# Performance work log

Measured on AMD Instinct MI355X. Metric: run time of the kernel, lower is better.

The kernel has to match this reference:

```python
import jax, jax.numpy as jnp
import numpy as np

B, T = 1024, 128
F_DIM, Z_DIM, TXT_DIM, H = 1024, 256, 768, 8
EPS = 1e-5


def layer_norm(x, g, b):
    mu = jnp.mean(x, axis=-1, keepdims=True)
    var = jnp.var(x, axis=-1, keepdims=True)
    return (x - mu) * jax.lax.rsqrt(var + EPS) * g + b


def setup_inputs() -> dict:
    key = jax.random.key(0)
    ks = jax.random.split(key, 16)
    s = lambda fi, fo: 1.0 / np.sqrt(fi)  # rough init scale
    inp = {
        "x": jax.random.normal(ks[0], (B, F_DIM), jnp.float32),
        "z": jax.random.normal(ks[1], (B, Z_DIM), jnp.float32),
        "text_feat": jax.random.normal(ks[2], (B, T, TXT_DIM), jnp.float32),
        "attention": jnp.ones((B, T), jnp.int32),
        # FiLM
        "Wg": jax.random.normal(ks[3], (F_DIM, Z_DIM), jnp.float32) * s(Z_DIM, F_DIM),
        "bg": jnp.zeros((F_DIM,), jnp.float32),
        "Wb": jax.random.normal(ks[4], (F_DIM, Z_DIM), jnp.float32) * s(Z_DIM, F_DIM),
        "bb": jnp.zeros((F_DIM,), jnp.float32),
        # Linear block (linear -> LayerNorm)
        "Wl": jax.random.normal(ks[5], (F_DIM, F_DIM), jnp.float32) * s(F_DIM, F_DIM),
        "bl": jnp.zeros((F_DIM,), jnp.float32),
        "ln1_g": jnp.ones((F_DIM,), jnp.float32),
        "ln1_b": jnp.zeros((F_DIM,), jnp.float32),
        # cross attention projections
        "Wq": jax.random.normal(ks[6], (F_DIM, F_DIM), jnp.float32) * s(F_DIM, F_DIM),
        "bq": jnp.zeros((F_DIM,), jnp.float32),
        "Wk": jax.random.normal(ks[7], (F_DIM, TXT_DIM), jnp.float32) * s(TXT_DIM, F_DIM),
        "bk": jnp.zeros((F_DIM,), jnp.float32),
        "Wv": jax.random.normal(ks[8], (F_DIM, TXT_DIM), jnp.float32) * s(TXT_DIM, F_DIM),
        "bv": jnp.zeros((F_DIM,), jnp.float32),
        "Wo": jax.random.normal(ks[9], (F_DIM, F_DIM), jnp.float32) * s(F_DIM, F_DIM),
        "bo": jnp.zeros((F_DIM,), jnp.float32),
        # post-attention LayerNorm
        "ln2_g": jnp.ones((F_DIM,), jnp.float32),
        "ln2_b": jnp.zeros((F_DIM,), jnp.float32),
    }
    return inp


def reference(x, z, text_feat, attention, Wg, bg, Wb, bb, Wl, bl, ln1_g, ln1_b,
              Wq, bq, Wk, bk, Wv, bv, Wo, bo, ln2_g, ln2_b):
    d = F_DIM // H
    # FiLM params from condition z
    gamma = z @ Wg.T + bg            # [B, F]
    beta = z @ Wb.T + bb             # [B, F]
    # Linear block: linear -> LayerNorm (dropout p=0, identity activation)
    out = layer_norm(x @ Wl.T + bl, ln1_g, ln1_b)
    out = out * (1.0 + gamma) + beta  # FiLM modulation
    # single-query multi-head cross attention
    q = (out @ Wq.T + bq).reshape(B, H, d)                 # [B, H, d] (query len 1)
    k = (text_feat @ Wk.T + bk).reshape(B, T, H, d)         # [B, T, H, d]
    v = (text_feat @ Wv.T + bv).reshape(B, T, H, d)
    scores = jnp.einsum("bhd,bthd->bht", q, k) / jnp.sqrt(jnp.float32(d))  # [B, H, T]
    mask = (attention[:, None, :] != 0)                     # [B, 1, T]
    scores = jnp.where(mask, scores, -jnp.inf)
    attn = jax.nn.softmax(scores, axis=-1)                  # [B, H, T]
    ctx = jnp.einsum("bht,bthd->bhd", attn, v).reshape(B, F_DIM)
    attn_out = ctx @ Wo.T + bo
    out = out + layer_norm(attn_out, ln2_g, ln2_b)
    return jax.nn.gelu(out, approximate=False)
```

## Files before the change

### kernel.cpp

```cpp
#include <hip/hip_runtime.h>

#define EPS 1e-5f

typedef __bf16 bf16x8 __attribute__((ext_vector_type(8)));
typedef float f32x4 __attribute__((ext_vector_type(4)));
typedef ushort ushort8 __attribute__((ext_vector_type(8)));

static __device__ __forceinline__ ushort f2bf(float x) {
    union { float f; unsigned u; } v; v.f = x;
    unsigned r = v.u + 0x7fffu + ((v.u >> 16) & 1u);
    return (ushort)(r >> 16);
}
static __device__ __forceinline__ float bf2f(ushort u) {
    union { unsigned u32; float f; } v; v.u32 = (unsigned)u << 16;
    return v.f;
}

template<int OB>
__global__ __launch_bounds__(256)
void gemm_bb(const ushort* __restrict__ A, int lda, int Aoffz,
             const ushort* __restrict__ W, int ldw, int Woffz,
             void* __restrict__ Cv, int ldc, int Coffz,
             const float* __restrict__ bias, int boffz,
             float scale, int K)
{
    const int z = blockIdx.z;
    A += (size_t)z * Aoffz;
    W += (size_t)z * Woffz;
    const int bm = blockIdx.y * 64, bn = blockIdx.x * 64;

    __shared__ ushort As[64][72];
    __shared__ ushort Bs[64][72];

    const int tid  = threadIdx.x;
    const int lane = tid & 63, wv = tid >> 6;
    const int wm = (wv >> 1) * 32, wn = (wv & 1) * 32;

    const int srow = tid >> 2;
    const int scol = (tid & 3) * 16;
    const ushort* Agp = A + (size_t)(bm + srow) * lda + scol;
    const ushort* Wgp = W + (size_t)(bn + srow) * ldw + scol;

    const int fr = lane & 15, fk = (lane >> 4) * 8;

    f32x4 acc[2][2] = {};

    ushort8 a0 = *(const ushort8*)(Agp);
    ushort8 a1 = *(const ushort8*)(Agp + 8);
    ushort8 b0 = *(const ushort8*)(Wgp);
    ushort8 b1 = *(const ushort8*)(Wgp + 8);

    for (int kt = 0; kt < K; kt += 64) {
        *(ushort8*)&As[srow][scol]     = a0;
        *(ushort8*)&As[srow][scol + 8] = a1;
        *(ushort8*)&Bs[srow][scol]     = b0;
        *(ushort8*)&Bs[srow][scol + 8] = b1;
        __syncthreads();
        if (kt + 64 < K) {
            a0 = *(const ushort8*)(Agp + kt + 64);
            a1 = *(const ushort8*)(Agp + kt + 64 + 8);
            b0 = *(const ushort8*)(Wgp + kt + 64);
            b1 = *(const ushort8*)(Wgp + kt + 64 + 8);
        }
        #pragma unroll
        for (int ks = 0; ks < 64; ks += 32) {
            bf16x8 af0 = *(const bf16x8*)&As[wm + fr][ks + fk];
            bf16x8 af1 = *(const bf16x8*)&As[wm + 16 + fr][ks + fk];
            bf16x8 bf0 = *(const bf16x8*)&Bs[wn + fr][ks + fk];
            bf16x8 bf1 = *(const bf16x8*)&Bs[wn + 16 + fr][ks + fk];
            acc[0][0] = __builtin_amdgcn_mfma_f32_16x16x32_bf16(af0, bf0, acc[0][0], 0, 0, 0);
            acc[0][1] = __builtin_amdgcn_mfma_f32_16x16x32_bf16(af0, bf1, acc[0][1], 0, 0, 0);
            acc[1][0] = __builtin_amdgcn_mfma_f32_16x16x32_bf16(af1, bf0, acc[1][0], 0, 0, 0);
            acc[1][1] = __builtin_amdgcn_mfma_f32_16x16x32_bf16(af1, bf1, acc[1][1], 0, 0, 0);
        }
        __syncthreads();
    }

    const int rbase = (lane >> 4) * 4;
    #pragma unroll
    for (int mi = 0; mi < 2; ++mi) {
        #pragma unroll
        for (int ni = 0; ni < 2; ++ni) {
            const int col = bn + wn + ni * 16 + fr;
            const float bvv = bias ? (bias + (size_t)z * boffz)[col] : 0.f;
            #pragma unroll
            for (int r = 0; r < 4; ++r) {
                const int row = bm + wm + mi * 16 + rbase + r;
                const float val = acc[mi][ni][r] * scale + bvv;
                if (OB) {
                    ((ushort*)Cv)[(size_t)z * Coffz + (size_t)row * ldc + col] = f2bf(val);
                } else {
                    ((float*)Cv)[(size_t)z * Coffz + (size_t)row * ldc + col] = val;
                }
            }
        }
    }
}

__global__ __launch_bounds__(256)
void cvt_all(const float* __restrict__ Wl, const float* __restrict__ Wq,
             const float* __restrict__ Wo, const float* __restrict__ Wv,
             const float* __restrict__ Wg, const float* __restrict__ Wb,
             const float* __restrict__ x,  const float* __restrict__ zc,
             const float* __restrict__ bg, const float* __restrict__ bb,
             ushort* __restrict__ WlB, ushort* __restrict__ WqB,
             ushort* __restrict__ WoB, ushort* __restrict__ WvB,
             ushort* __restrict__ WgbB, ushort* __restrict__ xB,
             ushort* __restrict__ zB, float* __restrict__ bgb)
{
    int gid = blockIdx.x * 256 + threadIdx.x;
    if (gid < 512) {
        f32x4 v = (gid < 256) ? *(const f32x4*)(bg + gid * 4)
                              : *(const f32x4*)(bb + (gid - 256) * 4);
        *(f32x4*)(bgb + gid * 4) = v;
    }
    const float* src; ushort* dst; int off;
    if      (gid <  262144) { src = Wl; dst = WlB;           off = gid;          }
    else if (gid <  524288) { src = Wq; dst = WqB;           off = gid - 262144; }
    else if (gid <  786432) { src = Wo; dst = WoB;           off = gid - 524288; }
    else if (gid <  983040) { src = Wv; dst = WvB;           off = gid - 786432; }
    else if (gid < 1048576) { src = Wg; dst = WgbB;          off = gid - 983040; }
    else if (gid < 1114112) { src = Wb; dst = WgbB + 262144; off = gid - 1048576;}
    else if (gid < 1376256) { src = x;  dst = xB;            off = gid - 1114112;}
    else if (gid < 1441792) { src = zc; dst = zB;            off = gid - 1376256;}
    else return;
    f32x4 v = *(const f32x4*)(src + (size_t)off * 4);
    ushort4 o;
    o.x = f2bf(v[0]); o.y = f2bf(v[1]); o.z = f2bf(v[2]); o.w = f2bf(v[3]);
    *(ushort4*)(dst + (size_t)off * 4) = o;
}

__global__ __launch_bounds__(256)
void transpose_wk(const float* __restrict__ Wk, ushort* __restrict__ WkT)
{
    __shared__ ushort s[32][33];
    const int h  = blockIdx.z;
    const int c0 = blockIdx.x * 32, d0 = blockIdx.y * 32;
    const int tx = threadIdx.x & 31, ty = threadIdx.x >> 5;
    #pragma unroll
    for (int i = 0; i < 4; ++i) {
        int d = d0 + ty + i * 8;
        s[ty + i * 8][tx] = f2bf(Wk[(size_t)(h * 128 + d) * 768 + c0 + tx]);
    }
    __syncthreads();
    #pragma unroll
    for (int i = 0; i < 4; ++i) {
        int c = c0 + ty + i * 8;
        WkT[((size_t)h * 768 + c) * 128 + d0 + tx] = s[tx][ty + i * 8];
    }
}

__device__ inline void block_reduce2(float& a, float& b, float* sred)
{
    #pragma unroll
    for (int off = 32; off; off >>= 1) {
        a += __shfl_xor(a, off);
        b += __shfl_xor(b, off);
    }
    int w = threadIdx.x >> 6, lane = threadIdx.x & 63;
    if (lane == 0) { sred[w * 2] = a; sred[w * 2 + 1] = b; }
    __syncthreads();
    a = sred[0] + sred[2] + sred[4] + sred[6];
    b = sred[1] + sred[3] + sred[5] + sred[7];
}

__global__ __launch_bounds__(256)
void rowops1(const float* __restrict__ h1, const float* __restrict__ gb,
             const float* __restrict__ g, const float* __restrict__ bta,
             ushort* __restrict__ outb)
{
    __shared__ float sred[8];
    int b = blockIdx.x, tid = threadIdx.x;
    const float4 v = ((const float4*)(h1 + (size_t)b * 1024))[tid];
    float s  = v.x + v.y + v.z + v.w;
    float ss = v.x * v.x + v.y * v.y + v.z * v.z + v.w * v.w;
    block_reduce2(s, ss, sred);
    float mu  = s * (1.f / 1024.f);
    float var = ss * (1.f / 1024.f) - mu * mu;
    float rs  = rsqrtf(var + EPS);
    float4 gv = ((const float4*)g)[tid];
    float4 bv = ((const float4*)bta)[tid];
    float4 ga = ((const float4*)(gb + (size_t)b * 2048))[tid];
    float4 be = ((const float4*)(gb + (size_t)b * 2048 + 1024))[tid];
    ushort4 o;
    o.x = f2bf(((v.x - mu) * rs * gv.x + bv.x) * (1.f + ga.x) + be.x);
    o.y = f2bf(((v.y - mu) * rs * gv.y + bv.y) * (1.f + ga.y) + be.y);
    o.z = f2bf(((v.z - mu) * rs * gv.z + bv.z) * (1.f + ga.z) + be.z);
    o.w = f2bf(((v.w - mu) * rs * gv.w + bv.w) * (1.f + ga.w) + be.w);
    ((ushort4*)(outb + (size_t)b * 1024))[tid] = o;
}

__global__ __launch_bounds__(256)
void rowops2(const ushort* __restrict__ outb, const float* __restrict__ ao,
             const float* __restrict__ g, const float* __restrict__ bta,
             float* __restrict__ dst)
{
    __shared__ float sred[8];
    int b = blockIdx.x, tid = threadIdx.x;
    const float4 v = ((const float4*)(ao + (size_t)b * 1024))[tid];
    float s  = v.x + v.y + v.z + v.w;
    float ss = v.x * v.x + v.y * v.y + v.z * v.z + v.w * v.w;
    block_reduce2(s, ss, sred);
    float mu  = s * (1.f / 1024.f);
    float var = ss * (1.f / 1024.f) - mu * mu;
    float rs  = rsqrtf(var + EPS);
    float4 gv = ((const float4*)g)[tid];
    float4 bv = ((const float4*)bta)[tid];
    ushort4 ou = ((const ushort4*)(outb + (size_t)b * 1024))[tid];
    float y0 = bf2f(ou.x) + ((v.x - mu) * rs * gv.x + bv.x);
    float y1 = bf2f(ou.y) + ((v.y - mu) * rs * gv.y + bv.y);
    float y2 = bf2f(ou.z) + ((v.z - mu) * rs * gv.z + bv.z);
    float y3 = bf2f(ou.w) + ((v.w - mu) * rs * gv.w + bv.w);
    float4 o;
    o.x = 0.5f * y0 * (1.f + erff(y0 * 0.70710678118654752f));
    o.y = 0.5f * y1 * (1.f + erff(y1 * 0.70710678118654752f));
    o.z = 0.5f * y2 * (1.f + erff(y2 * 0.70710678118654752f));
    o.w = 0.5f * y3 * (1.f + erff(y3 * 0.70710678118654752f));
    ((float4*)(dst + (size_t)b * 1024))[tid] = o;
}

__global__ __launch_bounds__(256)
void attn_fused(const float* __restrict__ tf, const ushort* __restrict__ qt,
                const int* __restrict__ att, ushort* __restrict__ ctxtf)
{
    const int b = blockIdx.x;
    const int tid = threadIdx.x, lane = tid & 63, wv = tid >> 6;

    __shared__ ushort qtS[16][776];
    __shared__ ushort TF[32][776];
    __shared__ float s_sc[8][32];
    __shared__ float ps[8][32];

    const float*  tfb = tf + (size_t)b * 98304;
    const ushort* qtb = qt + (size_t)b * 6144;

    {
        const int r  = tid >> 5;
        const int c0 = (tid & 31) * 24;
        #pragma unroll
        for (int j = 0; j < 3; ++j)
            *(ushort8*)&qtS[r][c0 + 8 * j] = *(const ushort8*)&qtb[r * 768 + c0 + 8 * j];
        const ushort8 z8 = {0,0,0,0,0,0,0,0};
        #pragma unroll
        for (int j = 0; j < 3; ++j)
            *(ushort8*)&qtS[8 + r][c0 + 8 * j] = z8;
    }

    float acc[2][3][4] = {};
    float mrun = -INFINITY, srun = 0.f;
    const int fr = lane & 15, fko = (lane >> 4) * 8;
    const int hloc = lane >> 5, tl = lane & 31;
    const int h_own = 2 * wv + hloc;
    const int h0 = 2 * wv;

    for (int s = 0; s < 4; ++s) {
        __syncthreads();
        {
            const int r  = tid >> 3;
            const int c0 = (tid & 7) * 96;
            const float* srcr = tfb + (size_t)(s * 32 + r) * 768 + c0;
            #pragma unroll
            for (int j = 0; j < 24; ++j) {
                f32x4 v = *(const f32x4*)(srcr + 4 * j);
                ushort4 o;
                o.x = f2bf(v[0]); o.y = f2bf(v[1]); o.z = f2bf(v[2]); o.w = f2bf(v[3]);
                *(ushort4*)&TF[r][c0 + 4 * j] = o;
            }
        }
        __syncthreads();
        if (wv < 2) {
            f32x4 sacc = {0.f, 0.f, 0.f, 0.f};
            #pragma unroll
            for (int ks = 0; ks < 768; ks += 32) {
                bf16x8 aq = *(const bf16x8*)&qtS[fr][ks + fko];
                bf16x8 bt = *(const bf16x8*)&TF[wv * 16 + fr][ks + fko];
                sacc = __builtin_amdgcn_mfma_f32_16x16x32_bf16(aq, bt, sacc, 0, 0, 0);
            }
            if (lane < 32) {
                const int hbase = (lane >> 4) * 4;
                #pragma unroll
                for (int r = 0; r < 4; ++r)
                    s_sc[hbase + r][wv * 16 + (lane & 15)] = sacc[r];
            }
        }
        __syncthreads();
        {
            const int mask = att[b * 128 + s * 32 + tl];
            float sv = mask ? s_sc[h_own][tl] : -INFINITY;
            float mx = sv;
            mx = fmaxf(mx, __shfl_xor(mx, 16));
            mx = fmaxf(mx, __shfl_xor(mx, 8));
            mx = fmaxf(mx, __shfl_xor(mx, 4));
            mx = fmaxf(mx, __shfl_xor(mx, 2));
            mx = fmaxf(mx, __shfl_xor(mx, 1));
            float mnew = fmaxf(mrun, mx);
            float p = mask ? __expf(sv - mnew) : 0.f;
            float f = (mnew == -INFINITY) ? 1.f : __expf(mrun - mnew);
            float psum = p;
            psum += __shfl_xor(psum, 16);
            psum += __shfl_xor(psum, 8);
            psum += __shfl_xor(psum, 4);
            psum += __shfl_xor(psum, 2);
            psum += __shfl_xor(psum, 1);
            srun = srun * f + psum;
            mrun = mnew;
            ps[h_own][tl] = p;
            const float f0 = __shfl(f, 0);
            const float f1 = __shfl(f, 32);
            #pragma unroll
            for (int k = 0; k < 3; ++k)
                #pragma unroll
                for (int e = 0; e < 4; ++e) {
                    acc[0][k][e] *= f0;
                    acc[1][k][e] *= f1;
                }
        }
        {
            #pragma unroll 8
            for (int t = 0; t < 32; ++t) {
                const float p0 = ps[h0][t];
                const float p1 = ps[h0 + 1][t];
                #pragma unroll
                for (int k = 0; k < 3; ++k) {
                    ushort4 u = *(const ushort4*)&TF[t][4 * lane + 256 * k];
                    float x0 = bf2f(u.x), x1 = bf2f(u.y), x2 = bf2f(u.z), x3 = bf2f(u.w);
                    acc[0][k][0] += p0 * x0; acc[0][k][1] += p0 * x1;
                    acc[0][k][2] += p0 * x2; acc[0][k][3] += p0 * x3;
                    acc[1][k][0] += p1 * x0; acc[1][k][1] += p1 * x1;
                    acc[1][k][2] += p1 * x2; acc[1][k][3] += p1 * x3;
                }
            }
        }
    }

    const float sum0 = __shfl(srun, 0);
    const float sum1 = __shfl(srun, 32);
    const float i0 = 1.f / sum0, i1 = 1.f / sum1;
    #pragma unroll
    for (int k = 0; k < 3; ++k) {
        ushort4 o0, o1;
        o0.x = f2bf(acc[0][k][0] * i0); o0.y = f2bf(acc[0][k][1] * i0);
        o0.z = f2bf(acc[0][k][2] * i0); o0.w = f2bf(acc[0][k][3] * i0);
        o1.x = f2bf(acc[1][k][0] * i1); o1.y = f2bf(acc[1][k][1] * i1);
        o1.z = f2bf(acc[1][k][2] * i1); o1.w = f2bf(acc[1][k][3] * i1);
        *(ushort4*)&ctxtf[(size_t)b * 6144 + (size_t)h0 * 768 + 4 * lane + 256 * k] = o0;
        *(ushort4*)&ctxtf[(size_t)b * 6144 + (size_t)(h0 + 1) * 768 + 4 * lane + 256 * k] = o1;
    }
}

extern "C" void kernel_launch(void* const* d_in, const int* in_sizes, int n_in,
                              void* d_out, int out_size, void* d_ws, size_t ws_size,
                              hipStream_t stream)
{
    const float* x    = (const float*)d_in[0];
    const float* zc   = (const float*)d_in[1];
    const float* tf   = (const float*)d_in[2];
    const int*   att  = (const int*)d_in[3];
    const float* Wg   = (const float*)d_in[4];
    const float* bg   = (const float*)d_in[5];
    const float* Wb   = (const float*)d_in[6];
    const float* bb   = (const float*)d_in[7];
    const float* Wl   = (const float*)d_in[8];
    const float* bl   = (const float*)d_in[9];
    const float* ln1g = (const float*)d_in[10];
    const float* ln1b = (const float*)d_in[11];
    const float* Wq   = (const float*)d_in[12];
    const float* bq   = (const float*)d_in[13];
    const float* Wk   = (const float*)d_in[14];
    const float* Wv   = (const float*)d_in[16];
    const float* bv   = (const float*)d_in[17];
    const float* Wo   = (const float*)d_in[18];
    const float* bo   = (const float*)d_in[19];
    const float* ln2g = (const float*)d_in[20];
    const float* ln2b = (const float*)d_in[21];

    float* ws = (float*)d_ws;
    const size_t M1 = 1u << 20;
    float* H1  = ws;
    float* GB  = ws + 1 * M1;
    float* AO  = ws + 3 * M1;
    float* bgb = ws + 4 * M1;

    ushort* u = (ushort*)(ws + 5 * M1);
    ushort* WlB  = u;
    ushort* WqB  = u + 1 * M1;
    ushort* WoB  = u + 2 * M1;
    ushort* WvB  = u + 3 * M1;
    ushort* WgbB = u + 3 * M1 + 786432;
    ushort* WkT  = u + 3 * M1 + 1310720;
    ushort* xB   = u + 5 * M1;
    ushort* zB   = u + 6 * M1;
    ushort* OUTB = u + 6 * M1 + 262144;
    ushort* Q    = u + 7 * M1 + 262144;
    ushort* QT   = u + 8 * M1 + 262144;
    ushort* CTXB = u + 14 * M1 + 262144;
    ushort* CTX  = u + 20 * M1 + 262144;

    dim3 blk(256);

    cvt_all<<<dim3(5632), blk, 0, stream>>>(Wl, Wq, Wo, Wv, Wg, Wb, x, zc, bg, bb,
                                            WlB, WqB, WoB, WvB, WgbB, xB, zB, bgb);
    transpose_wk<<<dim3(24, 4, 8), blk, 0, stream>>>(Wk, WkT);

    gemm_bb<0><<<dim3(16, 16, 1), blk, 0, stream>>>(xB, 1024, 0, WlB, 1024, 0,
        (void*)H1, 1024, 0, bl, 0, 1.f, 1024);
    gemm_bb<0><<<dim3(32, 16, 1), blk, 0, stream>>>(zB, 256, 0, WgbB, 256, 0,
        (void*)GB, 2048, 0, bgb, 0, 1.f, 256);
    rowops1<<<dim3(1024), blk, 0, stream>>>(H1, GB, ln1g, ln1b, OUTB);
    gemm_bb<1><<<dim3(16, 16, 1), blk, 0, stream>>>(OUTB, 1024, 0, WqB, 1024, 0,
        (void*)Q, 1024, 0, bq, 0, 1.f, 1024);
    gemm_bb<1><<<dim3(12, 16, 8), blk, 0, stream>>>(Q, 1024, 128, WkT, 128, 98304,
        (void*)QT, 6144, 768, nullptr, 0, 0.08838834764831845f, 128);
    attn_fused<<<dim3(1024), blk, 0, stream>>>(tf, QT, att, CTXB);
    gemm_bb<1><<<dim3(2, 16, 8), blk, 0, stream>>>(CTXB, 6144, 768, WvB, 768, 98304,
        (void*)CTX, 1024, 128, bv, 128, 1.f, 768);
    gemm_bb<0><<<dim3(16, 16, 1), blk, 0, stream>>>(CTX, 1024, 0, WoB, 1024, 0,
        (void*)AO, 1024, 0, bo, 0, 1.f, 1024);
    rowops2<<<dim3(1024), blk, 0, stream>>>(OUTB, AO, ln2g, ln2b, (float*)d_out);
}
```

Measured before the change: 673.8 us.

## Double K tile in GEMM, prefetch text chunks in attention, merge Wk transpose

The bf16 GEMM now stages a 128-wide K slice per iteration, which halves the number of barrier-separated iterations, at the cost of more LDS and registers. The attention kernel register-prefetches the next 32-row fp32 text_feat chunk while computing on the current one, so global loads overlap the MFMA work but about 96 extra registers stay live. The Wk transpose kernel is folded into cvt_all as extra blocks to save one launch.

```diff
diff --git a/kernel.cpp b/kernel.cpp
--- a/kernel.cpp
+++ b/kernel.cpp
@@ -29,15 +29,15 @@
     W += (size_t)z * Woffz;
     const int bm = blockIdx.y * 64, bn = blockIdx.x * 64;
 
-    __shared__ ushort As[64][72];
-    __shared__ ushort Bs[64][72];
+    __shared__ ushort As[64][136];
+    __shared__ ushort Bs[64][136];
 
     const int tid  = threadIdx.x;
     const int lane = tid & 63, wv = tid >> 6;
     const int wm = (wv >> 1) * 32, wn = (wv & 1) * 32;
 
     const int srow = tid >> 2;
-    const int scol = (tid & 3) * 16;
+    const int scol = (tid & 3) * 32;
     const ushort* Agp = A + (size_t)(bm + srow) * lda + scol;
     const ushort* Wgp = W + (size_t)(bn + srow) * ldw + scol;
 
@@ -45,25 +45,29 @@
 
     f32x4 acc[2][2] = {};
 
-    ushort8 a0 = *(const ushort8*)(Agp);
-    ushort8 a1 = *(const ushort8*)(Agp + 8);
-    ushort8 b0 = *(const ushort8*)(Wgp);
-    ushort8 b1 = *(const ushort8*)(Wgp + 8);
-
-    for (int kt = 0; kt < K; kt += 64) {
-        *(ushort8*)&As[srow][scol]     = a0;
-        *(ushort8*)&As[srow][scol + 8] = a1;
-        *(ushort8*)&Bs[srow][scol]     = b0;
-        *(ushort8*)&Bs[srow][scol + 8] = b1;
-        __syncthreads();
-        if (kt + 64 < K) {
-            a0 = *(const ushort8*)(Agp + kt + 64);
-            a1 = *(const ushort8*)(Agp + kt + 64 + 8);
-            b0 = *(const ushort8*)(Wgp + kt + 64);
-            b1 = *(const ushort8*)(Wgp + kt + 64 + 8);
-        }
-        #pragma unroll
-        for (int ks = 0; ks < 64; ks += 32) {
+    ushort8 a[4], b[4];
+    #pragma unroll
+    for (int j = 0; j < 4; ++j) {
+        a[j] = *(const ushort8*)(Agp + 8 * j);
+        b[j] = *(const ushort8*)(Wgp + 8 * j);
+    }
+
+    for (int kt = 0; kt < K; kt += 128) {
+        #pragma unroll
+        for (int j = 0; j < 4; ++j) {
+            *(ushort8*)&As[srow][scol + 8 * j] = a[j];
+            *(ushort8*)&Bs[srow][scol + 8 * j] = b[j];
+        }
+        __syncthreads();
+        if (kt + 128 < K) {
+            #pragma unroll
+            for (int j = 0; j < 4; ++j) {
+                a[j] = *(const ushort8*)(Agp + kt + 128 + 8 * j);
+                b[j] = *(const ushort8*)(Wgp + kt + 128 + 8 * j);
+            }
+        }
+        #pragma unroll
+        for (int ks = 0; ks < 128; ks += 32) {
             bf16x8 af0 = *(const bf16x8*)&As[wm + fr][ks + fk];
             bf16x8 af1 = *(const bf16x8*)&As[wm + 16 + fr][ks + fk];
             bf16x8 bf0 = *(const bf16x8*)&Bs[wn + fr][ks + fk];
@@ -103,12 +107,35 @@
              const float* __restrict__ Wg, const float* __restrict__ Wb,
              const float* __restrict__ x,  const float* __restrict__ zc,
              const float* __restrict__ bg, const float* __restrict__ bb,
+             const float* __restrict__ Wk,
              ushort* __restrict__ WlB, ushort* __restrict__ WqB,
              ushort* __restrict__ WoB, ushort* __restrict__ WvB,
              ushort* __restrict__ WgbB, ushort* __restrict__ xB,
-             ushort* __restrict__ zB, float* __restrict__ bgb)
-{
-    int gid = blockIdx.x * 256 + threadIdx.x;
+             ushort* __restrict__ zB, float* __restrict__ bgb,
+             ushort* __restrict__ WkT)
+{
+    __shared__ ushort s[32][33];
+    const int bx = blockIdx.x;
+    if (bx >= 5632) {
+        const int tb = bx - 5632;
+        const int h  = tb / 96;
+        const int rem = tb % 96;
+        const int c0 = (rem % 24) * 32, d0 = (rem / 24) * 32;
+        const int tx = threadIdx.x & 31, ty = threadIdx.x >> 5;
+        #pragma unroll
+        for (int i = 0; i < 4; ++i) {
+            int d = d0 + ty + i * 8;
+            s[ty + i * 8][tx] = f2bf(Wk[(size_t)(h * 128 + d) * 768 + c0 + tx]);
+        }
+        __syncthreads();
+        #pragma unroll
+        for (int i = 0; i < 4; ++i) {
+            int c = c0 + ty + i * 8;
+            WkT[((size_t)h * 768 + c) * 128 + d0 + tx] = s[tx][ty + i * 8];
+        }
+        return;
+    }
+    int gid = bx * 256 + threadIdx.x;
     if (gid < 512) {
         f32x4 v = (gid < 256) ? *(const f32x4*)(bg + gid * 4)
                               : *(const f32x4*)(bb + (gid - 256) * 4);
@@ -128,26 +155,6 @@
     ushort4 o;
     o.x = f2bf(v[0]); o.y = f2bf(v[1]); o.z = f2bf(v[2]); o.w = f2bf(v[3]);
     *(ushort4*)(dst + (size_t)off * 4) = o;
-}
-
-__global__ __launch_bounds__(256)
-void transpose_wk(const float* __restrict__ Wk, ushort* __restrict__ WkT)
-{
-    __shared__ ushort s[32][33];
-    const int h  = blockIdx.z;
-    const int c0 = blockIdx.x * 32, d0 = blockIdx.y * 32;
-    const int tx = threadIdx.x & 31, ty = threadIdx.x >> 5;
-    #pragma unroll
-    for (int i = 0; i < 4; ++i) {
-        int d = d0 + ty + i * 8;
-        s[ty + i * 8][tx] = f2bf(Wk[(size_t)(h * 128 + d) * 768 + c0 + tx]);
-    }
-    __syncthreads();
-    #pragma unroll
-    for (int i = 0; i < 4; ++i) {
-        int c = c0 + ty + i * 8;
-        WkT[((size_t)h * 768 + c) * 128 + d0 + tx] = s[tx][ty + i * 8];
-    }
 }
 
 __device__ inline void block_reduce2(float& a, float& b, float* sred)
@@ -253,21 +260,28 @@
     const int h_own = 2 * wv + hloc;
     const int h0 = 2 * wv;
 
+    const int pr  = tid >> 3;
+    const int pc0 = (tid & 7) * 96;
+    const float* srcp = tfb + (size_t)pr * 768 + pc0;
+    f32x4 pf[24];
+    #pragma unroll
+    for (int j = 0; j < 24; ++j) pf[j] = *(const f32x4*)(srcp + 4 * j);
+
     for (int s = 0; s < 4; ++s) {
         __syncthreads();
-        {
-            const int r  = tid >> 3;
-            const int c0 = (tid & 7) * 96;
-            const float* srcr = tfb + (size_t)(s * 32 + r) * 768 + c0;
+        #pragma unroll
+        for (int j = 0; j < 24; ++j) {
+            ushort4 o;
+            o.x = f2bf(pf[j][0]); o.y = f2bf(pf[j][1]);
+            o.z = f2bf(pf[j][2]); o.w = f2bf(pf[j][3]);
+            *(ushort4*)&TF[pr][pc0 + 4 * j] = o;
+        }
+        __syncthreads();
+        if (s < 3) {
+            const float* srcn = srcp + (size_t)(s + 1) * 32 * 768;
             #pragma unroll
-            for (int j = 0; j < 24; ++j) {
-                f32x4 v = *(const f32x4*)(srcr + 4 * j);
-                ushort4 o;
-                o.x = f2bf(v[0]); o.y = f2bf(v[1]); o.z = f2bf(v[2]); o.w = f2bf(v[3]);
-                *(ushort4*)&TF[r][c0 + 4 * j] = o;
-            }
-        }
-        __syncthreads();
+            for (int j = 0; j < 24; ++j) pf[j] = *(const f32x4*)(srcn + 4 * j);
+        }
         if (wv < 2) {
             f32x4 sacc = {0.f, 0.f, 0.f, 0.f};
             #pragma unroll
@@ -398,9 +412,8 @@
 
     dim3 blk(256);
 
-    cvt_all<<<dim3(5632), blk, 0, stream>>>(Wl, Wq, Wo, Wv, Wg, Wb, x, zc, bg, bb,
-                                            WlB, WqB, WoB, WvB, WgbB, xB, zB, bgb);
-    transpose_wk<<<dim3(24, 4, 8), blk, 0, stream>>>(Wk, WkT);
+    cvt_all<<<dim3(6400), blk, 0, stream>>>(Wl, Wq, Wo, Wv, Wg, Wb, x, zc, bg, bb, Wk,
+                                            WlB, WqB, WoB, WvB, WgbB, xB, zB, bgb, WkT);
 
     gemm_bb<0><<<dim3(16, 16, 1), blk, 0, stream>>>(xB, 1024, 0, WlB, 1024, 0,
         (void*)H1, 1024, 0, bl, 0, 1.f, 1024);
```

Result: no change. 673.8 us (+0.0%).
